# Performance work log

Measured on AMD Instinct MI355X. Metric: run time of the kernel, lower is better.

Reference implementation:

```python
import jax, jax.numpy as jnp
import numpy as np

N = 1_000_000   # number of scattered source rows
M = 50_000      # number of attention keys / segments
D = 128         # values_dim == keys_dim


def setup_inputs() -> dict:
    key = jax.random.key(0)
    k1, k2, k3, k4, k5 = jax.random.split(key, 5)
    scattered_values = jax.random.normal(k1, (N, D), dtype=jnp.float32)
    indices = jax.random.randint(k2, (N,), 0, M, dtype=jnp.int64)
    attn_keys = jax.random.normal(k3, (M, D), dtype=jnp.float32)
    W = jax.random.normal(k4, (D, D), dtype=jnp.float32) * (1.0 / np.sqrt(D))
    b = jax.random.normal(k5, (D,), dtype=jnp.float32) * 0.01
    return {"scattered_values": scattered_values, "indices": indices,
            "attn_keys": attn_keys, "W": W, "b": b}


def reference(scattered_values, indices, attn_keys, W, b):
    num_segments = attn_keys.shape[0]
    # linear key projection: [M, D]
    keys_proj = attn_keys @ W.T + b
    # gather projected keys per source row: [N, D]
    gathered = keys_proj[indices]
    # per-row dot-product score: [N]
    probs = jnp.sum(scattered_values * gathered, axis=1)
    # segment-wise (scatter) softmax over rows sharing the same index
    seg_max = jax.ops.segment_max(probs, indices, num_segments=num_segments)
    ex = jnp.exp(probs - seg_max[indices])
    seg_sum = jax.ops.segment_sum(ex, indices, num_segments=num_segments)
    scattered_scores = ex / seg_sum[indices]
    # scatter-sum of score-weighted values: [M, D]
    attn_applied = jax.ops.segment_sum(
        scattered_values * scattered_scores[:, None], indices,
        num_segments=num_segments)
    return scattered_scores, attn_applied
```

## Files before the change

kernel.cpp:

```cpp
#include <hip/hip_runtime.h>
#include <float.h>

#define D 128
#define CAP 512

__global__ __launch_bounds__(256) void k_keys_proj(
    const float* __restrict__ attn_keys, const float* __restrict__ W,
    const float* __restrict__ b, float* __restrict__ keys_proj, int M) {
  __shared__ float sKey[32][D + 1];
  __shared__ float sWt[32][D + 1];
  const int tid = threadIdx.x;
  const int tc = tid & 31;
  const int tr = tid >> 5;
  const int row0 = blockIdx.x * 32;

  for (int e = tid; e < 32 * D; e += 256) {
    int r = e >> 7, k = e & (D - 1);
    int row = row0 + r;
    sKey[r][k] = (row < M) ? attn_keys[(size_t)row * D + k] : 0.0f;
  }

  float acc[4][4];
#pragma unroll
  for (int i = 0; i < 4; ++i)
#pragma unroll
    for (int c = 0; c < 4; ++c) acc[i][c] = 0.0f;

  for (int kc = 0; kc < D; kc += 32) {
    __syncthreads();
    for (int e = tid; e < 32 * D; e += 256) {
      int k = e & 31, j = e >> 5;
      sWt[k][j] = W[(size_t)j * D + kc + k];
    }
    __syncthreads();
#pragma unroll 8
    for (int kk = 0; kk < 32; ++kk) {
      float kv[4], wv[4];
#pragma unroll
      for (int i = 0; i < 4; ++i) kv[i] = sKey[4 * tr + i][kc + kk];
#pragma unroll
      for (int c = 0; c < 4; ++c) wv[c] = sWt[kk][4 * tc + c];
#pragma unroll
      for (int i = 0; i < 4; ++i)
#pragma unroll
        for (int c = 0; c < 4; ++c) acc[i][c] += kv[i] * wv[c];
    }
  }

#pragma unroll
  for (int i = 0; i < 4; ++i) {
    int row = row0 + 4 * tr + i;
    if (row < M) {
#pragma unroll
      for (int c = 0; c < 4; ++c) {
        int j = 4 * tc + c;
        keys_proj[(size_t)row * D + j] = acc[i][c] + b[j];
      }
    }
  }
}

__global__ __launch_bounds__(256) void k_count(
    const int* __restrict__ indices, int* __restrict__ counts, int N) {
  int i = blockIdx.x * blockDim.x + threadIdx.x;
  const int stride = gridDim.x * blockDim.x;
  const int n4 = N >> 2;
  const int4* idx4 = (const int4*)indices;
  for (int j = i; j < n4; j += stride) {
    int4 v = idx4[j];
    atomicAdd(counts + v.x, 1);
    atomicAdd(counts + v.y, 1);
    atomicAdd(counts + v.z, 1);
    atomicAdd(counts + v.w, 1);
  }
  for (int j = (n4 << 2) + i; j < N; j += stride) atomicAdd(counts + indices[j], 1);
}

__global__ __launch_bounds__(256) void k_offsets(
    const int* __restrict__ counts, int* __restrict__ fillpos,
    int* __restrict__ cursor, int M) {
  int m = blockIdx.x * blockDim.x + threadIdx.x;
  if (m < M) fillpos[m] = atomicAdd(cursor, counts[m]);
}

__global__ __launch_bounds__(256) void k_fill(
    const int* __restrict__ indices, int* __restrict__ fillpos,
    int* __restrict__ rowids, int N) {
  int i = blockIdx.x * blockDim.x + threadIdx.x;
  const int stride = gridDim.x * blockDim.x;
  const int n4 = N >> 2;
  const int4* idx4 = (const int4*)indices;
  for (int j = i; j < n4; j += stride) {
    int4 v = idx4[j];
    int base = 4 * j;
    rowids[atomicAdd(fillpos + v.x, 1)] = base;
    rowids[atomicAdd(fillpos + v.y, 1)] = base + 1;
    rowids[atomicAdd(fillpos + v.z, 1)] = base + 2;
    rowids[atomicAdd(fillpos + v.w, 1)] = base + 3;
  }
  for (int j = (n4 << 2) + i; j < N; j += stride)
    rowids[atomicAdd(fillpos + indices[j], 1)] = j;
}

__global__ __launch_bounds__(256) void k_segment(
    const float* __restrict__ values, const int* __restrict__ rowids,
    const int* __restrict__ counts, const int* __restrict__ fillpos,
    const float* __restrict__ keys_proj, float* __restrict__ raw_ovf,
    float* __restrict__ scores, float* __restrict__ attn_out, int M) {
  __shared__ float sS[4][CAP];
  const int lane = threadIdx.x & 63;
  const int wv = threadIdx.x >> 6;
  const int m = blockIdx.x * 4 + wv;
  if (m >= M) return;
  const int g = lane >> 4;
  const int t = lane & 15;

  const int cnt = counts[m];
  const int start = fillpos[m] - cnt;

  const float4* kp = (const float4*)(keys_proj + (size_t)m * D);
  const float4 k1 = kp[2 * t], k2 = kp[2 * t + 1];
  const float4* vr = (const float4*)values;

  float run_m = -FLT_MAX, run_l = 0.0f;
  float4 accA = {0, 0, 0, 0}, accB = {0, 0, 0, 0};

  float4 a = {0, 0, 0, 0}, b = {0, 0, 0, 0};
  if (cnt > 0) {
    int id = rowids[start + min(g, cnt - 1)];
    a = vr[(size_t)id * 32 + 2 * t];
    b = vr[(size_t)id * 32 + 2 * t + 1];
  }

  for (int gb = 0; gb < cnt; gb += 4) {
    const float4 ca = a, cb = b;
    if (gb + 4 < cnt) {
      int nid = rowids[start + min(gb + 4 + g, cnt - 1)];
      a = vr[(size_t)nid * 32 + 2 * t];
      b = vr[(size_t)nid * 32 + 2 * t + 1];
    }
    float s = ca.x * k1.x + ca.y * k1.y + ca.z * k1.z + ca.w * k1.w +
              cb.x * k2.x + cb.y * k2.y + cb.z * k2.z + cb.w * k2.w;
    s += __shfl_xor(s, 1, 64);
    s += __shfl_xor(s, 2, 64);
    s += __shfl_xor(s, 4, 64);
    s += __shfl_xor(s, 8, 64);
    const float s0 = __shfl(s, 0, 64);
    const float s1 = __shfl(s, 16, 64);
    const float s2 = __shfl(s, 32, 64);
    const float s3 = __shfl(s, 48, 64);

    float al0, al1, al2, al3, p0, p1, p2, p3;
#define STEP(sj, actj, alj, pj)                                   \
    {                                                             \
      float ss = (actj) ? (sj) : -FLT_MAX;                        \
      float mn = fmaxf(run_m, ss);                                \
      alj = __expf(run_m - mn);                                   \
      pj = (actj) ? __expf(ss - mn) : 0.0f;                       \
      run_l = run_l * alj + pj;                                   \
      run_m = mn;                                                 \
    }
    STEP(s0, true, al0, p0);
    STEP(s1, gb + 1 < cnt, al1, p1);
    STEP(s2, gb + 2 < cnt, al2, p2);
    STEP(s3, gb + 3 < cnt, al3, p3);
#undef STEP
    const float f3 = 1.0f;
    const float f2 = al3;
    const float f1 = al3 * al2;
    const float f0 = f1 * al1;
    const float scale = f0 * al0;
    const float w = (g == 0) ? p0 * f0 : (g == 1) ? p1 * f1
                  : (g == 2) ? p2 * f2 : p3 * f3;
    accA.x = accA.x * scale + ca.x * w;
    accA.y = accA.y * scale + ca.y * w;
    accA.z = accA.z * scale + ca.z * w;
    accA.w = accA.w * scale + ca.w * w;
    accB.x = accB.x * scale + cb.x * w;
    accB.y = accB.y * scale + cb.y * w;
    accB.z = accB.z * scale + cb.z * w;
    accB.w = accB.w * scale + cb.w * w;

    if (lane == 0) {
      int r = gb;
      if (r < cnt) { if (r < CAP) sS[wv][r] = s0; else raw_ovf[start + r] = s0; }
      r = gb + 1;
      if (r < cnt) { if (r < CAP) sS[wv][r] = s1; else raw_ovf[start + r] = s1; }
      r = gb + 2;
      if (r < cnt) { if (r < CAP) sS[wv][r] = s2; else raw_ovf[start + r] = s2; }
      r = gb + 3;
      if (r < cnt) { if (r < CAP) sS[wv][r] = s3; else raw_ovf[start + r] = s3; }
    }
  }

#define RED(x) x += __shfl_xor(x, 16, 64); x += __shfl_xor(x, 32, 64)
  RED(accA.x); RED(accA.y); RED(accA.z); RED(accA.w);
  RED(accB.x); RED(accB.y); RED(accB.z); RED(accB.w);
#undef RED

  const float invl = (run_l > 0.0f) ? 1.0f / run_l : 0.0f;
  if (g == 0) {
    float4* op = (float4*)(attn_out + (size_t)m * D);
    float4 oA = {accA.x * invl, accA.y * invl, accA.z * invl, accA.w * invl};
    float4 oB = {accB.x * invl, accB.y * invl, accB.z * invl, accB.w * invl};
    op[2 * t] = oA;
    op[2 * t + 1] = oB;
  }

  for (int r = lane; r < cnt; r += 64) {
    const float s = (r < CAP) ? sS[wv][r] : raw_ovf[start + r];
    const int i = rowids[start + r];
    scores[i] = __expf(s - run_m) * invl;
  }
}

extern "C" void kernel_launch(void* const* d_in, const int* in_sizes, int n_in,
                              void* d_out, int out_size, void* d_ws, size_t ws_size,
                              hipStream_t stream) {
  const float* values = (const float*)d_in[0];
  const int* indices = (const int*)d_in[1];
  const float* attn_keys = (const float*)d_in[2];
  const float* W = (const float*)d_in[3];
  const float* b = (const float*)d_in[4];
  const int N = in_sizes[0] / D;
  const int M = in_sizes[2] / D;

  float* keys_proj = (float*)d_ws;
  int* counts = (int*)(keys_proj + (size_t)M * D);
  int* fillpos = counts + M;
  int* cursor = fillpos + M;
  int* rowids = cursor + 64;
  float* raw_ovf = (float*)(rowids + N);

  float* scores = (float*)d_out;
  float* attn_out = scores + N;

  hipMemsetAsync(counts, 0, (size_t)M * sizeof(int), stream);
  hipMemsetAsync(cursor, 0, 64 * sizeof(int), stream);

  k_keys_proj<<<(M + 31) / 32, 256, 0, stream>>>(attn_keys, W, b, keys_proj, M);
  k_count<<<1024, 256, 0, stream>>>(indices, counts, N);
  k_offsets<<<(M + 255) / 256, 256, 0, stream>>>(counts, fillpos, cursor, M);
  k_fill<<<1024, 256, 0, stream>>>(indices, fillpos, rowids, N);
  k_segment<<<(M + 3) / 4, 256, 0, stream>>>(values, rowids, counts, fillpos,
                                             keys_proj, raw_ovf, scores, attn_out, M);
}
```

Measured before the change: 882.0 us.

## Fuse key projection with counting; per-group online softmax with merge

```diff
diff --git a/kernel.cpp b/kernel.cpp
--- a/kernel.cpp
+++ b/kernel.cpp
@@ -4,12 +4,32 @@
 #define D 128
 #define CAP 512
 
-__global__ __launch_bounds__(256) void k_keys_proj(
+__global__ __launch_bounds__(256) void k_proj_count(
     const float* __restrict__ attn_keys, const float* __restrict__ W,
-    const float* __restrict__ b, float* __restrict__ keys_proj, int M) {
+    const float* __restrict__ bias, float* __restrict__ keys_proj, int M,
+    const int* __restrict__ indices, int* __restrict__ counts, int N,
+    int nProj) {
   __shared__ float sKey[32][D + 1];
   __shared__ float sWt[32][D + 1];
   const int tid = threadIdx.x;
+
+  if (blockIdx.x >= nProj) {
+    const int i = (blockIdx.x - nProj) * 256 + tid;
+    const int stride = 1024 * 256;
+    const int n4 = N >> 2;
+    const int4* idx4 = (const int4*)indices;
+    for (int j = i; j < n4; j += stride) {
+      int4 v = idx4[j];
+      atomicAdd(counts + v.x, 1);
+      atomicAdd(counts + v.y, 1);
+      atomicAdd(counts + v.z, 1);
+      atomicAdd(counts + v.w, 1);
+    }
+    for (int j = (n4 << 2) + i; j < N; j += stride)
+      atomicAdd(counts + indices[j], 1);
+    return;
+  }
+
   const int tc = tid & 31;
   const int tr = tid >> 5;
   const int row0 = blockIdx.x * 32;
@@ -54,26 +74,10 @@
 #pragma unroll
       for (int c = 0; c < 4; ++c) {
         int j = 4 * tc + c;
-        keys_proj[(size_t)row * D + j] = acc[i][c] + b[j];
+        keys_proj[(size_t)row * D + j] = acc[i][c] + bias[j];
       }
     }
   }
-}
-
-__global__ __launch_bounds__(256) void k_count(
-    const int* __restrict__ indices, int* __restrict__ counts, int N) {
-  int i = blockIdx.x * blockDim.x + threadIdx.x;
-  const int stride = gridDim.x * blockDim.x;
-  const int n4 = N >> 2;
-  const int4* idx4 = (const int4*)indices;
-  for (int j = i; j < n4; j += stride) {
-    int4 v = idx4[j];
-    atomicAdd(counts + v.x, 1);
-    atomicAdd(counts + v.y, 1);
-    atomicAdd(counts + v.z, 1);
-    atomicAdd(counts + v.w, 1);
-  }
-  for (int j = (n4 << 2) + i; j < N; j += stride) atomicAdd(counts + indices[j], 1);
 }
 
 __global__ __launch_bounds__(256) void k_offsets(
@@ -119,25 +123,26 @@
   const int start = fillpos[m] - cnt;
 
   const float4* kp = (const float4*)(keys_proj + (size_t)m * D);
-  const float4 k1 = kp[2 * t], k2 = kp[2 * t + 1];
+  const float4 k1 = kp[t];
+  const float4 k2 = kp[t + 16];
   const float4* vr = (const float4*)values;
 
   float run_m = -FLT_MAX, run_l = 0.0f;
   float4 accA = {0, 0, 0, 0}, accB = {0, 0, 0, 0};
 
-  float4 a = {0, 0, 0, 0}, b = {0, 0, 0, 0};
+  float4 a = {0, 0, 0, 0}, bb = {0, 0, 0, 0};
   if (cnt > 0) {
     int id = rowids[start + min(g, cnt - 1)];
-    a = vr[(size_t)id * 32 + 2 * t];
-    b = vr[(size_t)id * 32 + 2 * t + 1];
+    a = vr[(size_t)id * 32 + t];
+    bb = vr[(size_t)id * 32 + 16 + t];
   }
 
   for (int gb = 0; gb < cnt; gb += 4) {
-    const float4 ca = a, cb = b;
+    const float4 ca = a, cb = bb;
     if (gb + 4 < cnt) {
       int nid = rowids[start + min(gb + 4 + g, cnt - 1)];
-      a = vr[(size_t)nid * 32 + 2 * t];
-      b = vr[(size_t)nid * 32 + 2 * t + 1];
+      a = vr[(size_t)nid * 32 + t];
+      bb = vr[(size_t)nid * 32 + 16 + t];
     }
     float s = ca.x * k1.x + ca.y * k1.y + ca.z * k1.z + ca.w * k1.w +
               cb.x * k2.x + cb.y * k2.y + cb.z * k2.z + cb.w * k2.w;
@@ -145,66 +150,60 @@
     s += __shfl_xor(s, 2, 64);
     s += __shfl_xor(s, 4, 64);
     s += __shfl_xor(s, 8, 64);
-    const float s0 = __shfl(s, 0, 64);
-    const float s1 = __shfl(s, 16, 64);
-    const float s2 = __shfl(s, 32, 64);
-    const float s3 = __shfl(s, 48, 64);
-
-    float al0, al1, al2, al3, p0, p1, p2, p3;
-#define STEP(sj, actj, alj, pj)                                   \
-    {                                                             \
-      float ss = (actj) ? (sj) : -FLT_MAX;                        \
-      float mn = fmaxf(run_m, ss);                                \
-      alj = __expf(run_m - mn);                                   \
-      pj = (actj) ? __expf(ss - mn) : 0.0f;                       \
-      run_l = run_l * alj + pj;                                   \
-      run_m = mn;                                                 \
-    }
-    STEP(s0, true, al0, p0);
-    STEP(s1, gb + 1 < cnt, al1, p1);
-    STEP(s2, gb + 2 < cnt, al2, p2);
-    STEP(s3, gb + 3 < cnt, al3, p3);
-#undef STEP
-    const float f3 = 1.0f;
-    const float f2 = al3;
-    const float f1 = al3 * al2;
-    const float f0 = f1 * al1;
-    const float scale = f0 * al0;
-    const float w = (g == 0) ? p0 * f0 : (g == 1) ? p1 * f1
-                  : (g == 2) ? p2 * f2 : p3 * f3;
-    accA.x = accA.x * scale + ca.x * w;
-    accA.y = accA.y * scale + ca.y * w;
-    accA.z = accA.z * scale + ca.z * w;
-    accA.w = accA.w * scale + ca.w * w;
-    accB.x = accB.x * scale + cb.x * w;
-    accB.y = accB.y * scale + cb.y * w;
-    accB.z = accB.z * scale + cb.z * w;
-    accB.w = accB.w * scale + cb.w * w;
-
-    if (lane == 0) {
-      int r = gb;
-      if (r < cnt) { if (r < CAP) sS[wv][r] = s0; else raw_ovf[start + r] = s0; }
-      r = gb + 1;
-      if (r < cnt) { if (r < CAP) sS[wv][r] = s1; else raw_ovf[start + r] = s1; }
-      r = gb + 2;
-      if (r < cnt) { if (r < CAP) sS[wv][r] = s2; else raw_ovf[start + r] = s2; }
-      r = gb + 3;
-      if (r < cnt) { if (r < CAP) sS[wv][r] = s3; else raw_ovf[start + r] = s3; }
-    }
-  }
-
-#define RED(x) x += __shfl_xor(x, 16, 64); x += __shfl_xor(x, 32, 64)
-  RED(accA.x); RED(accA.y); RED(accA.z); RED(accA.w);
-  RED(accB.x); RED(accB.y); RED(accB.z); RED(accB.w);
-#undef RED
+    const bool act = (gb + g) < cnt;
+    const float mn = act ? fmaxf(run_m, s) : run_m;
+    const float al = __expf(run_m - mn);
+    const float p = act ? __expf(s - mn) : 0.0f;
+    run_l = run_l * al + p;
+    run_m = mn;
+    accA.x = accA.x * al + ca.x * p;
+    accA.y = accA.y * al + ca.y * p;
+    accA.z = accA.z * al + ca.z * p;
+    accA.w = accA.w * al + ca.w * p;
+    accB.x = accB.x * al + cb.x * p;
+    accB.y = accB.y * al + cb.y * p;
+    accB.z = accB.z * al + cb.z * p;
+    accB.w = accB.w * al + cb.w * p;
+    if (t == 0 && act) {
+      int r = gb + g;
+      if (r < CAP) sS[wv][r] = s; else raw_ovf[start + r] = s;
+    }
+  }
+
+#pragma unroll
+  for (int off = 16; off < 64; off <<= 1) {
+    float om = __shfl_xor(run_m, off, 64);
+    float ol = __shfl_xor(run_l, off, 64);
+    float ax = __shfl_xor(accA.x, off, 64);
+    float ay = __shfl_xor(accA.y, off, 64);
+    float az = __shfl_xor(accA.z, off, 64);
+    float aw = __shfl_xor(accA.w, off, 64);
+    float bx = __shfl_xor(accB.x, off, 64);
+    float by = __shfl_xor(accB.y, off, 64);
+    float bz = __shfl_xor(accB.z, off, 64);
+    float bw = __shfl_xor(accB.w, off, 64);
+    const float mn = fmaxf(run_m, om);
+    const float ea = __expf(run_m - mn);
+    const float eb = __expf(om - mn);
+    run_l = run_l * ea + ol * eb;
+    accA.x = accA.x * ea + ax * eb;
+    accA.y = accA.y * ea + ay * eb;
+    accA.z = accA.z * ea + az * eb;
+    accA.w = accA.w * ea + aw * eb;
+    accB.x = accB.x * ea + bx * eb;
+    accB.y = accB.y * ea + by * eb;
+    accB.z = accB.z * ea + bz * eb;
+    accB.w = accB.w * ea + bw * eb;
+    run_m = mn;
+  }
 
   const float invl = (run_l > 0.0f) ? 1.0f / run_l : 0.0f;
   if (g == 0) {
     float4* op = (float4*)(attn_out + (size_t)m * D);
     float4 oA = {accA.x * invl, accA.y * invl, accA.z * invl, accA.w * invl};
     float4 oB = {accB.x * invl, accB.y * invl, accB.z * invl, accB.w * invl};
-    op[2 * t] = oA;
-    op[2 * t + 1] = oB;
+    op[t] = oA;
+    op[t + 16] = oB;
   }
 
   for (int r = lane; r < cnt; r += 64) {
@@ -238,8 +237,9 @@
   hipMemsetAsync(counts, 0, (size_t)M * sizeof(int), stream);
   hipMemsetAsync(cursor, 0, 64 * sizeof(int), stream);
 
-  k_keys_proj<<<(M + 31) / 32, 256, 0, stream>>>(attn_keys, W, b, keys_proj, M);
-  k_count<<<1024, 256, 0, stream>>>(indices, counts, N);
+  const int nProj = (M + 31) / 32;
+  k_proj_count<<<nProj + 1024, 256, 0, stream>>>(attn_keys, W, b, keys_proj, M,
+                                                 indices, counts, N, nProj);
   k_offsets<<<(M + 255) / 256, 256, 0, stream>>>(counts, fillpos, cursor, M);
   k_fill<<<1024, 256, 0, stream>>>(indices, fillpos, rowids, N);
   k_segment<<<(M + 3) / 4, 256, 0, stream>>>(values, rowids, counts, fillpos,
```

Result: faster. 863.1 us (-2.1%).
